# Optimization experiments

Measured on AMD Instinct MI355X. Metric: run time of the kernel, lower is better.

The kernel has to match this reference:

```python
import jax, jax.numpy as jnp
import numpy as np

N = 40000          # nodes
E = 640000         # edges (avg degree 16)
IN_F = 128
OUT_F = 128
DIST_DIM = 32
N_BOUND = 32       # embedding table has N_BOUND+1 rows


def _xavier(key, shape):
    fan_in, fan_out = shape
    std = (2.0 / (fan_in + fan_out)) ** 0.5
    return jax.random.normal(key, shape, jnp.float32) * std


def setup_inputs() -> dict:
    key = jax.random.key(0)
    ks = jax.random.split(key, 12)
    feat = jax.random.normal(ks[0], (N, IN_F), jnp.float32)
    loc = jax.random.uniform(ks[1], (N, 2), jnp.float32) * 10.0
    src = jax.random.randint(ks[2], (E,), 0, N)
    dst = jax.random.randint(ks[3], (E,), 0, N)
    inter_ids = jax.random.randint(ks[4], (E,), 0, N)
    # weights stored [in, out] (torch Linear weight transposed)
    W_fc = _xavier(ks[5], (IN_F, OUT_F))
    Wq = _xavier(ks[6], (OUT_F, OUT_F))
    Wk = _xavier(ks[7], (OUT_F, OUT_F))
    Wq2 = _xavier(ks[8], (2 * OUT_F, OUT_F))
    Wk2 = _xavier(ks[9], (2 * OUT_F, OUT_F))
    G_w = _xavier(ks[10], (DIST_DIM, OUT_F))
    embed = jax.random.normal(ks[11], (N_BOUND + 1, DIST_DIM), jnp.float32)
    boundaries = jnp.linspace(0.45, 14.4, N_BOUND).astype(jnp.float32)
    return dict(feat=feat, loc=loc, W_fc=W_fc, Wq=Wq, Wk=Wk, Wq2=Wq2,
                Wk2=Wk2, G_w=G_w, embed=embed, boundaries=boundaries,
                src=src, dst=dst, inter_ids=inter_ids)


def reference(feat, loc, W_fc, Wq, Wk, Wq2, Wk2, G_w, embed, boundaries,
              src, dst, inter_ids):
    scale = jnp.sqrt(jnp.float32(OUT_F))
    h = feat @ W_fc                               # [N, OUT_F]  (feat_h)

    f_src = feat[src]                             # [E, IN_F]
    f_dst = feat[dst]                             # [E, IN_F]

    # attention score e1 (the only score the source module actually uses)
    q = f_dst @ Wq                                # [E, OUT_F]
    k = f_src @ Wk                                # [E, OUT_F]
    e = jnp.sum(q * k, axis=1) / scale            # [E]

    # --- e2 branch: computed by the source but discarded (returns only 'e': e1).
    # Reproduced for fidelity; XLA dead-code-eliminates it.
    inter_pos = loc[inter_ids]
    dist1 = jnp.linalg.norm(loc[dst] - loc[src], axis=1)
    dist_ = jnp.linalg.norm(loc[src] - inter_pos, axis=1)
    de1 = embed[jnp.searchsorted(boundaries, dist1, side='left')] @ G_w
    de_ = embed[jnp.searchsorted(boundaries, dist_, side='left')] @ G_w
    q2 = jnp.concatenate([f_src, de1], axis=1) @ Wq2
    k2 = jnp.concatenate([feat[inter_ids], de_], axis=1) @ Wk2
    _e2 = jnp.sum(q2 * k2, axis=1) / scale        # unused, as in source
    # ---

    # edge_softmax: segmented softmax over incoming edges of each dst node
    e_max = jax.ops.segment_max(e, dst, num_segments=N)      # [N]
    ex = jnp.exp(e - e_max[dst])                              # [E]
    denom = jax.ops.segment_sum(ex, dst, num_segments=N)     # [N]
    a = ex / denom[dst]                                       # [E]

    # u_mul_e + sum: out[v] = sum_{(u->v)} h[u] * a_uv
    msgs = h[src] * a[:, None]                                # [E, OUT_F]
    rst = jax.ops.segment_sum(msgs, dst, num_segments=N)     # [N, OUT_F]
    return rst
```

## Files before the change

kernel.cpp:

```cpp
#include <hip/hip_runtime.h>
#include <hip/hip_bf16.h>

#define NN 40000
#define NE 640000

typedef __attribute__((ext_vector_type(4))) float f32x4;
typedef __attribute__((ext_vector_type(8))) short bf16x8;

__device__ inline float bflo(unsigned int w) { return __uint_as_float(w << 16); }
__device__ inline float bfhi(unsigned int w) { return __uint_as_float(w & 0xffff0000u); }
__device__ inline unsigned short f2bf(float x) {
  __hip_bfloat16 b = __float2bfloat16(x);
  return *(unsigned short*)&b;
}

__global__ __launch_bounds__(256) void k0_prep(const float* __restrict__ w0,
                                               const float* __restrict__ w1,
                                               const float* __restrict__ w2,
                                               unsigned short* __restrict__ Wt,
                                               int* __restrict__ pos) {
  const int b = blockIdx.x, t = threadIdx.x;
  if (b < 3) {
    const float* w = (b == 0) ? w0 : (b == 1) ? w1 : w2;
    unsigned short* o = Wt + b * 16384;
    for (int idx = t; idx < 16384; idx += 256) {
      int k = idx >> 7, c = idx & 127;
      o[c * 128 + k] = f2bf(w[idx]);
    }
  } else {
    ((int4*)pos)[(b - 3) * 256 + t] = (int4){0, 0, 0, 0};
  }
}

__global__ __launch_bounds__(256) void k1_gemm_fill(const float* __restrict__ feat,
                                                    const unsigned short* __restrict__ wt_all,
                                                    unsigned short* __restrict__ Qb,
                                                    unsigned short* __restrict__ KH,
                                                    const int* __restrict__ src,
                                                    const int* __restrict__ dst,
                                                    int* __restrict__ pos,
                                                    int* __restrict__ csr) {
  const int bid = blockIdx.x, t = threadIdx.x;

  if (bid < 2048) {
    const int g = bid & 7;
    const int blk = bid >> 3;
    const int vlo = g * 5000, vhi = vlo + 5000;
    for (int c = blk; c < 2500; c += 256) {
      const int e = c * 256 + t;
      const int v = dst[e];
      if (v >= vlo && v < vhi) {
        const int slot = atomicAdd(&pos[v], 1);
        if (slot < 64) csr[v * 64 + slot] = src[e];
      }
    }
    return;
  }

  __shared__ unsigned short sA[64][136];
  __shared__ unsigned short sB[128][136];
  const int gi = bid - 2048;
  const int by = gi / 625, bx = gi % 625;
  const unsigned short* wt = wt_all + by * 16384;
  const int rbase = bx * 64;

  const float4* fa = (const float4*)(feat + (size_t)rbase * 128);
  #pragma unroll
  for (int j = 0; j < 8; ++j) {
    int idx = t + j * 256;
    float4 v = fa[idx];
    ushort4 r;
    r.x = f2bf(v.x); r.y = f2bf(v.y); r.z = f2bf(v.z); r.w = f2bf(v.w);
    *(ushort4*)&sA[idx >> 5][(idx & 31) << 2] = r;
  }
  const uint4* wb = (const uint4*)wt;
  #pragma unroll
  for (int j = 0; j < 8; ++j) {
    int idx = t + j * 256;
    uint4 v = wb[idx];
    *(uint4*)&sB[idx >> 4][(idx & 15) << 3] = v;
  }
  __syncthreads();

  const int l = t & 63;
  const int w = t >> 6;
  const int r16 = l & 15;
  const int kb = (l >> 4) << 3;
  f32x4 acc[8];
  #pragma unroll
  for (int ch = 0; ch < 8; ++ch) acc[ch] = (f32x4){0.f, 0.f, 0.f, 0.f};

  #pragma unroll
  for (int ks = 0; ks < 4; ++ks) {
    const int k0 = ks * 32 + kb;
    bf16x8 a = *(const bf16x8*)&sA[w * 16 + r16][k0];
    #pragma unroll
    for (int ch = 0; ch < 8; ++ch) {
      bf16x8 b = *(const bf16x8*)&sB[ch * 16 + r16][k0];
      acc[ch] = __builtin_amdgcn_mfma_f32_16x16x32_bf16(a, b, acc[ch], 0, 0, 0);
    }
  }
  const int orow = rbase + w * 16 + ((l >> 4) << 2);
  const int ocol = l & 15;
  const float scl = (by == 1) ? 0.08838834764831845f : 1.0f;
  unsigned short* ob;
  int stride, off;
  if (by == 1) { ob = Qb; stride = 128; off = 0; }
  else         { ob = KH; stride = 256; off = (by == 0) ? 128 : 0; }
  #pragma unroll
  for (int ch = 0; ch < 8; ++ch) {
    #pragma unroll
    for (int r = 0; r < 4; ++r) {
      ob[(size_t)(orow + r) * stride + off + ch * 16 + ocol] = f2bf(acc[ch][r] * scl);
    }
  }
}

__global__ __launch_bounds__(256) void node_k(const char* __restrict__ Qb,
                                              const char* __restrict__ KH,
                                              const int* __restrict__ deg,
                                              const int* __restrict__ csr,
                                              float* __restrict__ out) {
  const int v = blockIdx.x * 4 + (threadIdx.x >> 6);
  const int l = threadIdx.x & 63;
  const int g = l >> 4;
  const int i = l & 15;

  const uint4 qw = *(const uint4*)(Qb + (size_t)v * 256 + i * 16);
  float qf[8];
  qf[0] = bflo(qw.x); qf[1] = bfhi(qw.x); qf[2] = bflo(qw.y); qf[3] = bfhi(qw.y);
  qf[4] = bflo(qw.z); qf[5] = bfhi(qw.z); qf[6] = bflo(qw.w); qf[7] = bfhi(qw.w);

  int d_ = deg[v];
  d_ = (d_ > 64) ? 64 : d_;
  const int* cbase = csr + v * 64;

  float den = 0.f;
  float acc[8];
  #pragma unroll
  for (int j = 0; j < 8; ++j) acc[j] = 0.f;

  #pragma unroll
  for (int t = 0; t < 16; ++t) {
    const int eidx = 4 * t + g;
    if (eidx < d_) {
      const int u = cbase[eidx];
      const char* row = KH + (size_t)u * 512;
      const uint4 kw = *(const uint4*)(row + i * 16);
      const uint4 hw = *(const uint4*)(row + 256 + i * 16);
      float s = qf[0] * bflo(kw.x) + qf[1] * bfhi(kw.x)
              + qf[2] * bflo(kw.y) + qf[3] * bfhi(kw.y)
              + qf[4] * bflo(kw.z) + qf[5] * bfhi(kw.z)
              + qf[6] * bflo(kw.w) + qf[7] * bfhi(kw.w);
      s += __shfl_xor(s, 1); s += __shfl_xor(s, 2);
      s += __shfl_xor(s, 4); s += __shfl_xor(s, 8);
      const float p = __expf(s);
      den += p;
      acc[0] += p * bflo(hw.x); acc[1] += p * bfhi(hw.x);
      acc[2] += p * bflo(hw.y); acc[3] += p * bfhi(hw.y);
      acc[4] += p * bflo(hw.z); acc[5] += p * bfhi(hw.z);
      acc[6] += p * bflo(hw.w); acc[7] += p * bfhi(hw.w);
    }
  }

  #pragma unroll
  for (int off = 16; off < 64; off <<= 1) {
    den += __shfl_xor(den, off);
    #pragma unroll
    for (int j = 0; j < 8; ++j) acc[j] += __shfl_xor(acc[j], off);
  }

  if (g == 0) {
    const float inv = (d_ > 0) ? 1.0f / den : 0.f;
    float4 r0, r1;
    r0.x = acc[0] * inv; r0.y = acc[1] * inv; r0.z = acc[2] * inv; r0.w = acc[3] * inv;
    r1.x = acc[4] * inv; r1.y = acc[5] * inv; r1.z = acc[6] * inv; r1.w = acc[7] * inv;
    float* ob = out + (size_t)v * 128 + i * 8;
    *(float4*)ob = r0;
    *(float4*)(ob + 4) = r1;
  }
}

extern "C" void kernel_launch(void* const* d_in, const int* in_sizes, int n_in,
                              void* d_out, int out_size, void* d_ws, size_t ws_size,
                              hipStream_t stream) {
  const float* feat = (const float*)d_in[0];
  const float* W_fc = (const float*)d_in[2];
  const float* Wq   = (const float*)d_in[3];
  const float* Wk   = (const float*)d_in[4];
  const int* src = (const int*)d_in[10];
  const int* dst = (const int*)d_in[11];

  char* ws = (char*)d_ws;
  unsigned short* Wt = (unsigned short*)(ws);
  unsigned short* Qb = (unsigned short*)(ws + 98304);
  unsigned short* KH = (unsigned short*)(ws + 10338304);
  int* pos = (int*)(ws + 30818304);
  int* csr = (int*)(ws + 30982144);

  k0_prep<<<43, 256, 0, stream>>>(W_fc, Wq, Wk, Wt, pos);
  k1_gemm_fill<<<3923, 256, 0, stream>>>(feat, Wt, Qb, KH, src, dst, pos, csr);
  node_k<<<10000, 256, 0, stream>>>((const char*)Qb, (const char*)KH,
                                    pos, csr, (float*)d_out);
}
```

Before: 199.7 us.

## Restructure projection GEMM to reuse feat fragments across three weights without LDS

The GEMM blocks now load each node row's feat once into registers as MFMA B-fragments and loop over all three weight matrices. Weight fragments are read straight from global/L2 and the outputs are stored transposed, so each lane writes packed ushort4 values. This removes the LDS staging, the barrier and the threefold re-read and re-conversion of feat. The CSR fill also moves from range-partitioned strided blocks to one edge per thread, which brings back atomic contention across the whole node range. The cost is heavier weight traffic through the cache, now read by every block.

```diff
diff --git a/kernel.cpp b/kernel.cpp
--- a/kernel.cpp
+++ b/kernel.cpp
@@ -42,76 +42,57 @@
                                                     int* __restrict__ csr) {
   const int bid = blockIdx.x, t = threadIdx.x;
 
-  if (bid < 2048) {
-    const int g = bid & 7;
-    const int blk = bid >> 3;
-    const int vlo = g * 5000, vhi = vlo + 5000;
-    for (int c = blk; c < 2500; c += 256) {
-      const int e = c * 256 + t;
-      const int v = dst[e];
-      if (v >= vlo && v < vhi) {
-        const int slot = atomicAdd(&pos[v], 1);
-        if (slot < 64) csr[v * 64 + slot] = src[e];
-      }
-    }
+  if (bid < 2500) {
+    const int e = bid * 256 + t;
+    const int v = dst[e];
+    const int slot = atomicAdd(&pos[v], 1);
+    if (slot < 64) csr[v * 64 + slot] = src[e];
     return;
   }
 
-  __shared__ unsigned short sA[64][136];
-  __shared__ unsigned short sB[128][136];
-  const int gi = bid - 2048;
-  const int by = gi / 625, bx = gi % 625;
-  const unsigned short* wt = wt_all + by * 16384;
-  const int rbase = bx * 64;
+  const int bx = bid - 2500;
+  const int l = t & 63, w = t >> 6;
+  const int r16 = l & 15, kb = l >> 4;
+  const int node = bx * 64 + w * 16 + r16;
 
-  const float4* fa = (const float4*)(feat + (size_t)rbase * 128);
+  bf16x8 bfr[4];
+  const float* fb = feat + (size_t)node * 128 + kb * 8;
   #pragma unroll
-  for (int j = 0; j < 8; ++j) {
-    int idx = t + j * 256;
-    float4 v = fa[idx];
-    ushort4 r;
-    r.x = f2bf(v.x); r.y = f2bf(v.y); r.z = f2bf(v.z); r.w = f2bf(v.w);
-    *(ushort4*)&sA[idx >> 5][(idx & 31) << 2] = r;
+  for (int ks = 0; ks < 4; ++ks) {
+    const float4 p0 = *(const float4*)(fb + ks * 32);
+    const float4 p1 = *(const float4*)(fb + ks * 32 + 4);
+    bf16x8 a;
+    a[0] = (short)f2bf(p0.x); a[1] = (short)f2bf(p0.y);
+    a[2] = (short)f2bf(p0.z); a[3] = (short)f2bf(p0.w);
+    a[4] = (short)f2bf(p1.x); a[5] = (short)f2bf(p1.y);
+    a[6] = (short)f2bf(p1.z); a[7] = (short)f2bf(p1.w);
+    bfr[ks] = a;
   }
-  const uint4* wb = (const uint4*)wt;
-  #pragma unroll
-  for (int j = 0; j < 8; ++j) {
-    int idx = t + j * 256;
-    uint4 v = wb[idx];
-    *(uint4*)&sB[idx >> 4][(idx & 15) << 3] = v;
-  }
-  __syncthreads();
-
-  const int l = t & 63;
-  const int w = t >> 6;
-  const int r16 = l & 15;
-  const int kb = (l >> 4) << 3;
-  f32x4 acc[8];
-  #pragma unroll
-  for (int ch = 0; ch < 8; ++ch) acc[ch] = (f32x4){0.f, 0.f, 0.f, 0.f};
 
   #pragma unroll
-  for (int ks = 0; ks < 4; ++ks) {
-    const int k0 = ks * 32 + kb;
-    bf16x8 a = *(const bf16x8*)&sA[w * 16 + r16][k0];
+  for (int m = 0; m < 3; ++m) {
+    const unsigned short* wtm = wt_all + m * 16384;
+    f32x4 acc[8];
     #pragma unroll
-    for (int ch = 0; ch < 8; ++ch) {
-      bf16x8 b = *(const bf16x8*)&sB[ch * 16 + r16][k0];
-      acc[ch] = __builtin_amdgcn_mfma_f32_16x16x32_bf16(a, b, acc[ch], 0, 0, 0);
+    for (int tt = 0; tt < 8; ++tt) acc[tt] = (f32x4){0.f, 0.f, 0.f, 0.f};
+    #pragma unroll
+    for (int ks = 0; ks < 4; ++ks) {
+      #pragma unroll
+      for (int tt = 0; tt < 8; ++tt) {
+        const bf16x8 afr = *(const bf16x8*)(wtm + (tt * 16 + r16) * 128 + ks * 32 + kb * 8);
+        acc[tt] = __builtin_amdgcn_mfma_f32_16x16x32_bf16(afr, bfr[ks], acc[tt], 0, 0, 0);
+      }
     }
-  }
-  const int orow = rbase + w * 16 + ((l >> 4) << 2);
-  const int ocol = l & 15;
-  const float scl = (by == 1) ? 0.08838834764831845f : 1.0f;
-  unsigned short* ob;
-  int stride, off;
-  if (by == 1) { ob = Qb; stride = 128; off = 0; }
-  else         { ob = KH; stride = 256; off = (by == 0) ? 128 : 0; }
-  #pragma unroll
-  for (int ch = 0; ch < 8; ++ch) {
+    const float scl = (m == 1) ? 0.08838834764831845f : 1.0f;
     #pragma unroll
-    for (int r = 0; r < 4; ++r) {
-      ob[(size_t)(orow + r) * stride + off + ch * 16 + ocol] = f2bf(acc[ch][r] * scl);
+    for (int tt = 0; tt < 8; ++tt) {
+      const int oc = tt * 16 + kb * 4;
+      ushort4 pk;
+      pk.x = f2bf(acc[tt][0] * scl); pk.y = f2bf(acc[tt][1] * scl);
+      pk.z = f2bf(acc[tt][2] * scl); pk.w = f2bf(acc[tt][3] * scl);
+      if (m == 1)      *(ushort4*)(Qb + (size_t)node * 128 + oc) = pk;
+      else if (m == 0) *(ushort4*)(KH + (size_t)node * 256 + 128 + oc) = pk;
+      else             *(ushort4*)(KH + (size_t)node * 256 + oc) = pk;
     }
   }
 }
@@ -199,7 +180,7 @@
   int* csr = (int*)(ws + 30982144);
 
   k0_prep<<<43, 256, 0, stream>>>(W_fc, Wq, Wk, Wt, pos);
-  k1_gemm_fill<<<3923, 256, 0, stream>>>(feat, Wt, Qb, KH, src, dst, pos, csr);
+  k1_gemm_fill<<<3125, 256, 0, stream>>>(feat, Wt, Qb, KH, src, dst, pos, csr);
   node_k<<<10000, 256, 0, stream>>>((const char*)Qb, (const char*)KH,
                                     pos, csr, (float*)d_out);
 }
```

Result: slower. 238.7 us (+19.5%).

## Fuse weight transpose into GEMM blocks and interleave CSR-fill blocks

Applied to the files above, without the earlier changes.

Removes the separate prep kernel: each GEMM block now converts and transposes its fp32 weight matrix into shared memory itself, and the degree counters are zeroed with hipMemsetAsync. CSR-fill work is split into one 256-edge chunk per block without the per-group range filter, and fill blocks are interleaved 4:3 with GEMM blocks so the atomic-bound fill and the MFMA GEMM share the GPU at the same time. node_k gets a launch-bounds occupancy hint. Trade-offs: every GEMM block redundantly reads 64KB of fp32 weights and does scattered 2-byte transposed LDS writes, and unfiltered atomics lose the locality the old per-range grouping gave.

```diff
diff --git a/kernel.cpp b/kernel.cpp
--- a/kernel.cpp
+++ b/kernel.cpp
@@ -14,26 +14,10 @@
   return *(unsigned short*)&b;
 }
 
-__global__ __launch_bounds__(256) void k0_prep(const float* __restrict__ w0,
-                                               const float* __restrict__ w1,
-                                               const float* __restrict__ w2,
-                                               unsigned short* __restrict__ Wt,
-                                               int* __restrict__ pos) {
-  const int b = blockIdx.x, t = threadIdx.x;
-  if (b < 3) {
-    const float* w = (b == 0) ? w0 : (b == 1) ? w1 : w2;
-    unsigned short* o = Wt + b * 16384;
-    for (int idx = t; idx < 16384; idx += 256) {
-      int k = idx >> 7, c = idx & 127;
-      o[c * 128 + k] = f2bf(w[idx]);
-    }
-  } else {
-    ((int4*)pos)[(b - 3) * 256 + t] = (int4){0, 0, 0, 0};
-  }
-}
-
 __global__ __launch_bounds__(256) void k1_gemm_fill(const float* __restrict__ feat,
-                                                    const unsigned short* __restrict__ wt_all,
+                                                    const float* __restrict__ w0,
+                                                    const float* __restrict__ w1,
+                                                    const float* __restrict__ w2,
                                                     unsigned short* __restrict__ Qb,
                                                     unsigned short* __restrict__ KH,
                                                     const int* __restrict__ src,
@@ -41,49 +25,47 @@
                                                     int* __restrict__ pos,
                                                     int* __restrict__ csr) {
   const int bid = blockIdx.x, t = threadIdx.x;
+  const int r7 = bid % 7, k7 = bid / 7;
 
-  if (bid < 2048) {
-    const int g = bid & 7;
-    const int blk = bid >> 3;
-    const int vlo = g * 5000, vhi = vlo + 5000;
-    for (int c = blk; c < 2500; c += 256) {
-      const int e = c * 256 + t;
-      const int v = dst[e];
-      if (v >= vlo && v < vhi) {
-        const int slot = atomicAdd(&pos[v], 1);
-        if (slot < 64) csr[v * 64 + slot] = src[e];
-      }
-    }
+  if (r7 < 4) {
+    const int e = (k7 * 4 + r7) * 256 + t;
+    const int v = dst[e];
+    const int slot = atomicAdd(&pos[v], 1);
+    if (slot < 64) csr[v * 64 + slot] = src[e];
     return;
   }
 
   __shared__ unsigned short sA[64][136];
   __shared__ unsigned short sB[128][136];
-  const int gi = bid - 2048;
+  const int gi = k7 * 3 + (r7 - 4);
   const int by = gi / 625, bx = gi % 625;
-  const unsigned short* wt = wt_all + by * 16384;
   const int rbase = bx * 64;
+  const float* w = (by == 0) ? w0 : (by == 1) ? w1 : w2;
 
+  #pragma unroll
+  for (int j = 0; j < 16; ++j) {
+    const int fi = j * 256 + t;
+    const float4 v = ((const float4*)w)[fi];
+    const int k = fi >> 5;
+    const int c = (fi & 31) << 2;
+    sB[c + 0][k] = f2bf(v.x);
+    sB[c + 1][k] = f2bf(v.y);
+    sB[c + 2][k] = f2bf(v.z);
+    sB[c + 3][k] = f2bf(v.w);
+  }
   const float4* fa = (const float4*)(feat + (size_t)rbase * 128);
   #pragma unroll
   for (int j = 0; j < 8; ++j) {
-    int idx = t + j * 256;
-    float4 v = fa[idx];
+    const int idx = t + j * 256;
+    const float4 v = fa[idx];
     ushort4 r;
     r.x = f2bf(v.x); r.y = f2bf(v.y); r.z = f2bf(v.z); r.w = f2bf(v.w);
     *(ushort4*)&sA[idx >> 5][(idx & 31) << 2] = r;
   }
-  const uint4* wb = (const uint4*)wt;
-  #pragma unroll
-  for (int j = 0; j < 8; ++j) {
-    int idx = t + j * 256;
-    uint4 v = wb[idx];
-    *(uint4*)&sB[idx >> 4][(idx & 15) << 3] = v;
-  }
   __syncthreads();
 
   const int l = t & 63;
-  const int w = t >> 6;
+  const int wv = t >> 6;
   const int r16 = l & 15;
   const int kb = (l >> 4) << 3;
   f32x4 acc[8];
@@ -93,14 +75,14 @@
   #pragma unroll
   for (int ks = 0; ks < 4; ++ks) {
     const int k0 = ks * 32 + kb;
-    bf16x8 a = *(const bf16x8*)&sA[w * 16 + r16][k0];
+    bf16x8 a = *(const bf16x8*)&sA[wv * 16 + r16][k0];
     #pragma unroll
     for (int ch = 0; ch < 8; ++ch) {
       bf16x8 b = *(const bf16x8*)&sB[ch * 16 + r16][k0];
       acc[ch] = __builtin_amdgcn_mfma_f32_16x16x32_bf16(a, b, acc[ch], 0, 0, 0);
     }
   }
-  const int orow = rbase + w * 16 + ((l >> 4) << 2);
+  const int orow = rbase + wv * 16 + ((l >> 4) << 2);
   const int ocol = l & 15;
   const float scl = (by == 1) ? 0.08838834764831845f : 1.0f;
   unsigned short* ob;
@@ -116,11 +98,11 @@
   }
 }
 
-__global__ __launch_bounds__(256) void node_k(const char* __restrict__ Qb,
-                                              const char* __restrict__ KH,
-                                              const int* __restrict__ deg,
-                                              const int* __restrict__ csr,
-                                              float* __restrict__ out) {
+__global__ __launch_bounds__(256, 8) void node_k(const char* __restrict__ Qb,
+                                                 const char* __restrict__ KH,
+                                                 const int* __restrict__ deg,
+                                                 const int* __restrict__ csr,
+                                                 float* __restrict__ out) {
   const int v = blockIdx.x * 4 + (threadIdx.x >> 6);
   const int l = threadIdx.x & 63;
   const int g = l >> 4;
@@ -192,14 +174,13 @@
   const int* dst = (const int*)d_in[11];
 
   char* ws = (char*)d_ws;
-  unsigned short* Wt = (unsigned short*)(ws);
-  unsigned short* Qb = (unsigned short*)(ws + 98304);
-  unsigned short* KH = (unsigned short*)(ws + 10338304);
-  int* pos = (int*)(ws + 30818304);
-  int* csr = (int*)(ws + 30982144);
+  unsigned short* Qb = (unsigned short*)(ws);
+  unsigned short* KH = (unsigned short*)(ws + 10240000);
+  int* pos = (int*)(ws + 30720000);
+  int* csr = (int*)(ws + 30880000);
 
-  k0_prep<<<43, 256, 0, stream>>>(W_fc, Wq, Wk, Wt, pos);
-  k1_gemm_fill<<<3923, 256, 0, stream>>>(feat, Wt, Qb, KH, src, dst, pos, csr);
+  (void)hipMemsetAsync(pos, 0, NN * sizeof(int), stream);
+  k1_gemm_fill<<<4375, 256, 0, stream>>>(feat, W_fc, Wq, Wk, Qb, KH, src, dst, pos, csr);
   node_k<<<10000, 256, 0, stream>>>((const char*)Qb, (const char*)KH,
                                     pos, csr, (float*)d_out);
 }
```

After: 178.9 us. 1.12x faster.
